# Kernel optimization log

Measured on AMD Instinct MI355X. Metric: run time of the kernel, lower is better.

## Reference

```python
import jax, jax.numpy as jnp
import numpy as np

BS, SL, H, DE, DT = 32, 512, 1024, 1024, 64


def setup_inputs() -> dict:
    key = jax.random.key(0)
    ks = jax.random.split(key, 12)
    cas_emb = jax.random.normal(ks[0], (BS, SL, DE), jnp.float32)
    # prefix (length) mask: position i valid iff i < length_b
    lengths = jax.random.randint(ks[1], (BS,), SL // 4, SL + 1)
    cas_mask = (jnp.arange(SL)[None, :] < lengths[:, None]).astype(jnp.float32)[..., None]
    time_weight = jax.random.uniform(ks[2], (BS, SL, DT), jnp.float32)
    s = 0.02
    return {
        "cas_emb": cas_emb,
        "cas_mask": cas_mask,
        "time_weight": time_weight,
        "W1": jax.random.normal(ks[3], (DE, H), jnp.float32) * s,
        "b1": jnp.zeros((H,), jnp.float32),
        "Wh": jax.random.normal(ks[4], (H, H), jnp.float32) * s,
        "bh": jnp.zeros((H,), jnp.float32),
        "Wt": jax.random.normal(ks[5], (H, H), jnp.float32) * s,
        "bt": jnp.zeros((H,), jnp.float32),
        "Wg": jax.random.normal(ks[6], (2 * H, H), jnp.float32) * s,
        "bg": jnp.zeros((H,), jnp.float32),
        "Wm1": jax.random.normal(ks[7], (H, H), jnp.float32) * s,
        "bm1": jnp.zeros((H,), jnp.float32),
        "Wti": jax.random.normal(ks[8], (DT, H), jnp.float32) * s,
        "bti": jnp.zeros((H,), jnp.float32),
        "Wm2": jax.random.normal(ks[9], (H, 1), jnp.float32) * s,
        "bm2": jnp.zeros((1,), jnp.float32),
    }


def reference(cas_emb, cas_mask, time_weight, W1, b1, Wh, bh, Wt, bt, Wg, bg,
              Wm1, bm1, Wti, bti, Wm2, bm2):
    NEG = jnp.float32(-1e30)
    sl = cas_emb.shape[1]
    # --- user2user: directional masked self-attention + fusion gate ---
    # attention_mask[b,i,j] = (i > j) and cas_mask[b,j]
    direction = (jnp.arange(sl)[:, None] > jnp.arange(sl)[None, :])  # [sl,sl]
    attn_mask = (direction[None] & (cas_mask[..., 0][:, None, :] > 0)).astype(cas_emb.dtype)  # [bs,sl,sl]
    cas_hidden = jax.nn.elu(cas_emb @ W1 + b1) * cas_mask  # [bs,sl,H]
    head = cas_hidden @ Wh + bh
    tail = cas_hidden @ Wt + bt
    logits = jnp.einsum('bih,bjh->bij', head, tail) + (1.0 - attn_mask) * NEG
    score = jax.nn.softmax(logits, axis=-1) * attn_mask  # renormalized-masked softmax
    depend = jnp.einsum('bij,bjh->bih', score, cas_hidden)
    gate = jax.nn.sigmoid(jnp.concatenate([cas_hidden, depend], axis=-1) @ Wg + bg)
    encoding = (gate * cas_hidden + (1.0 - gate) * depend) * cas_mask  # [bs,sl,H]
    # --- user2cas: time-weighted attention pooling ---
    map1 = jax.nn.elu(encoding @ Wm1 + bm1)
    time_inf = jax.nn.elu(time_weight @ Wti + bti)
    map2 = (map1 * time_inf) @ Wm2 + bm2  # [bs,sl,1]
    a = jax.nn.softmax(map2 + NEG * (1.0 - cas_mask), axis=1) * cas_mask
    return a * encoding
```

## Files before the change

### kernel.cpp

```cpp
#include <hip/hip_runtime.h>
#include <math.h>


#define BSZ 32
#define SLEN 512
#define HD 1024
#define DEMB 1024
#define DTW 64

typedef __attribute__((ext_vector_type(8))) short short8;
typedef __attribute__((ext_vector_type(4))) float f32x4;
typedef unsigned short ushort_t;

__device__ __forceinline__ unsigned short f2bf(float x) {
    unsigned int u = __float_as_uint(x);
    u += 0x7FFFu + ((u >> 16) & 1u);
    return (unsigned short)(u >> 16);
}
__device__ __forceinline__ float bf2f(unsigned short h) {
    return __uint_as_float(((unsigned int)h) << 16);
}

__device__ __forceinline__ void gload16(const void* g, void* l) {
    __builtin_amdgcn_global_load_lds((const __attribute__((address_space(1))) unsigned int*)g,
                                     (__attribute__((address_space(3))) unsigned int*)l,
                                     16, 0, 0);
}

template<int ACT, int MSK, int ACC, int WF32, int WBF16, int MODE, int EPI,
         int KCAP = 0, int SKIP = 0>
__global__ __launch_bounds__(256, 4)
void mgemm(const ushort_t* __restrict__ AH, const ushort_t* __restrict__ AL,
           long long ldA, long long bsA,
           const ushort_t* __restrict__ BH, const ushort_t* __restrict__ BL,
           long long ldB, long long bsB,
           const float* __restrict__ bias, const float* __restrict__ rowmask,
           long long mskb,
           float* __restrict__ C, long long ldC, long long bsC,
           ushort_t* __restrict__ OH, ushort_t* __restrict__ OL,
           long long ldO, long long bsO,
           int M, int N, int K,
           const float* __restrict__ f_tinf, const float* __restrict__ f_wm2,
           float* __restrict__ f_out)
{
    __shared__ alignas(16) ushort_t sAh[128 * 32];
    __shared__ alignas(16) ushort_t sAl[128 * 32];
    __shared__ alignas(16) ushort_t sBh[128 * 32];
    __shared__ alignas(16) ushort_t sBl[128 * 32];

    long long bz = blockIdx.z;
    int tid = threadIdx.x;
    int wv = tid >> 6, lane = tid & 63;
    int wr = wv >> 1, wc = wv & 1;
    int ln = lane & 15, qd = lane >> 4;

    int bx = blockIdx.x, by = blockIdx.y;
    if (MODE == 1) {
        int G = gridDim.x;
        int L = by * G + bx;
        int X = L & 7, S = L >> 3;
        bx = S % G;
        int t = S / G;
        by = ((t >> 1) * 8 + X) * 2 + (t & 1);
    }
    if (MODE == 2) {
        int l = blockIdx.x;
        if (l < 1)      { by = 0; bx = 0; }
        else if (l < 3) { by = 1; bx = l - 1; }
        else if (l < 6) { by = 2; bx = l - 3; }
        else            { by = 3; bx = l - 6; }
    }
    long long m0 = (long long)by * 128;
    long long n0 = (long long)bx * 128;

    if (SKIP) {
        int alive = __syncthreads_or(
            (tid < 128) && (rowmask[bz * mskb + m0 + tid] != 0.f));
        if (alive == 0) {
            if (SKIP == 1) {
                if (EPI == 2 || WBF16) {
                    ushort_t* OHb = OH + bz * bsO;
                    ushort_t* OLb = OL + bz * bsO;
                    short8 z = {};
                    #pragma unroll
                    for (int p = 0; p < 8; ++p) {
                        int idx = tid + p * 256;
                        long long o = (m0 + (idx >> 4)) * ldO + n0 + (idx & 15) * 8;
                        *(short8*)&OHb[o] = z;
                        *(short8*)&OLb[o] = z;
                    }
                }
                if (WF32) {
                    float* Cb = C + bz * bsC;
                    float4 z = make_float4(0.f, 0.f, 0.f, 0.f);
                    #pragma unroll
                    for (int p = 0; p < 16; ++p) {
                        int idx = tid + p * 256;
                        *(float4*)&Cb[(m0 + (idx >> 5)) * ldC + n0 + (idx & 31) * 4] = z;
                    }
                }
            }
            return;
        }
    }

    const ushort_t* gsrc;
    ushort_t* ldst;
    long long gld;
    if (wv == 0)      { gsrc = AH + bz * bsA + (m0 + (lane >> 2)) * ldA; ldst = sAh; gld = ldA; }
    else if (wv == 1) { gsrc = AL + bz * bsA + (m0 + (lane >> 2)) * ldA; ldst = sAl; gld = ldA; }
    else if (wv == 2) { gsrc = BH + bz * bsB + (n0 + (lane >> 2)) * ldB; ldst = sBh; gld = ldB; }
    else              { gsrc = BL + bz * bsB + (n0 + (lane >> 2)) * ldB; ldst = sBl; gld = ldB; }
    gsrc += (lane & 3) * 8;

    f32x4 acc[4][4] = {};

    int KL = K;
    if (KCAP) {
        long long kc = m0 + 128;
        if (kc < (long long)KL) KL = (int)kc;
    }

    for (int k0 = 0; k0 < KL; k0 += 32) {
        #pragma unroll
        for (int i = 0; i < 8; ++i)
            gload16(gsrc + (long long)(16 * i) * gld + k0, ldst + i * 512);
        __syncthreads();

        short8 fah[4], fal[4], fbh[4], fbl[4];
        #pragma unroll
        for (int i = 0; i < 4; ++i) {
            int ra = (64 * wr + 16 * i + ln) * 32 + qd * 8;
            int rb = (64 * wc + 16 * i + ln) * 32 + qd * 8;
            fah[i] = *(const short8*)&sAh[ra];
            fal[i] = *(const short8*)&sAl[ra];
            fbh[i] = *(const short8*)&sBh[rb];
            fbl[i] = *(const short8*)&sBl[rb];
        }
        #pragma unroll
        for (int i = 0; i < 4; ++i)
            #pragma unroll
            for (int j = 0; j < 4; ++j) {
                acc[i][j] = __builtin_amdgcn_mfma_f32_16x16x32_bf16(fah[i], fbh[j], acc[i][j], 0, 0, 0);
                acc[i][j] = __builtin_amdgcn_mfma_f32_16x16x32_bf16(fah[i], fbl[j], acc[i][j], 0, 0, 0);
                acc[i][j] = __builtin_amdgcn_mfma_f32_16x16x32_bf16(fal[i], fbh[j], acc[i][j], 0, 0, 0);
            }
        __syncthreads();
    }

    if (EPI == 1) {
        int Ni = N;
        #pragma unroll
        for (int i = 0; i < 4; ++i) {
            #pragma unroll
            for (int t = 0; t < 4; ++t) {
                int gm = (int)m0 + 64 * wr + 16 * i + qd * 4 + t;
                int tb = gm * Ni + (int)n0 + 64 * wc + ln;
                float part = 0.f;
                #pragma unroll
                for (int j = 0; j < 4; ++j) {
                    int gn = (int)n0 + 64 * wc + 16 * j + ln;
                    float x = acc[i][j][t] + bias[gn];
                    x = (x > 0.f) ? x : (expf(x) - 1.f);
                    part += x * f_tinf[tb + 16 * j] * f_wm2[gn];
                }
                part += __shfl_xor(part, 1);
                part += __shfl_xor(part, 2);
                part += __shfl_xor(part, 4);
                part += __shfl_xor(part, 8);
                if (ln == 0) atomicAdd(&f_out[gm], part);
            }
        }
        return;
    }

    if (EPI == 2) {
        int ldCi = (int)ldC, ldOi = (int)ldO, ldAi = (int)ldA;
        int nb = (int)n0 + 64 * wc + ln;
        #pragma unroll
        for (int i = 0; i < 4; ++i) {
            #pragma unroll
            for (int t = 0; t < 4; ++t) {
                int gm = (int)m0 + 64 * wr + 16 * i + qd * 4 + t;
                float mk = rowmask[gm];
                int cb = gm * ldCi + nb;
                int ob = gm * ldOi + nb;
                int ab = gm * ldAi + nb;
                #pragma unroll
                for (int j = 0; j < 4; ++j) {
                    float x = acc[i][j][t] + C[cb + 16 * j];
                    float g = 1.f / (1.f + expf(-x));
                    int o = ob + 16 * j;
                    float c = bf2f(OH[o]) + bf2f(OL[o]);
                    int ai = ab + 16 * j;
                    float d = bf2f(AH[ai]) + bf2f(AL[ai]);
                    float r = (g * c + (1.f - g) * d) * mk;
                    unsigned short h = f2bf(r);
                    OH[o] = h;
                    OL[o] = f2bf(r - bf2f(h));
                }
            }
        }
        return;
    }

    float* Cb = 0;
    ushort_t *OHb = 0, *OLb = 0;
    if (WF32 || ACC) Cb = C + bz * bsC;
    if (WBF16) { OHb = OH + bz * bsO; OLb = OL + bz * bsO; }

    #pragma unroll
    for (int i = 0; i < 4; ++i) {
        #pragma unroll
        for (int t = 0; t < 4; ++t) {
            long long gm = m0 + 64 * wr + 16 * i + qd * 4 + t;
            float mk = 1.f;
            if (MSK) mk = rowmask[gm];
            #pragma unroll
            for (int j = 0; j < 4; ++j) {
                long long gn = n0 + 64 * wc + 16 * j + ln;
                float x = acc[i][j][t];
                if (bias) x += bias[gn];
                if (ACC) x += Cb[gm * ldC + gn];
                if (ACT) x = (x > 0.f) ? x : (expf(x) - 1.f);
                if (MSK) x *= mk;
                if (WF32 || ACC) Cb[gm * ldC + gn] = x;
                if (WBF16) {
                    unsigned short h = f2bf(x);
                    OHb[gm * ldO + gn] = h;
                    OLb[gm * ldO + gn] = f2bf(x - bf2f(h));
                }
            }
        }
    }
}


__global__ __launch_bounds__(256)
void zero_k(float* __restrict__ p, long long n)
{
    long long i = blockIdx.x * 256LL + threadIdx.x;
    if (i < n) p[i] = 0.f;
}

__global__ __launch_bounds__(256)
void split_k(const float* __restrict__ x, ushort_t* __restrict__ h,
             ushort_t* __restrict__ l, long long n4)
{
    long long i = blockIdx.x * 256LL + threadIdx.x;
    long long stride = (long long)gridDim.x * 256LL;
    for (; i < n4; i += stride) {
        float4 v = ((const float4*)x)[i];
        ushort4 hv, lv;
        hv.x = f2bf(v.x); lv.x = f2bf(v.x - bf2f(hv.x));
        hv.y = f2bf(v.y); lv.y = f2bf(v.y - bf2f(hv.y));
        hv.z = f2bf(v.z); lv.z = f2bf(v.z - bf2f(hv.z));
        hv.w = f2bf(v.w); lv.w = f2bf(v.w - bf2f(hv.w));
        ((ushort4*)h)[i] = hv;
        ((ushort4*)l)[i] = lv;
    }
}

__global__ __launch_bounds__(256)
void tsplit_k(const float* __restrict__ X,
              ushort_t* __restrict__ Th, ushort_t* __restrict__ Tl,
              int K, int N)
{
    __shared__ float t[32][33];
    int n0 = blockIdx.x * 32, k0 = blockIdx.y * 32;
    int tx = threadIdx.x & 31, ty = threadIdx.x >> 5;
    #pragma unroll
    for (int p = 0; p < 32; p += 8)
        t[ty + p][tx] = X[(long long)(k0 + ty + p) * N + n0 + tx];
    __syncthreads();
    #pragma unroll
    for (int p = 0; p < 32; p += 8) {
        float v = t[tx][ty + p];
        unsigned short h = f2bf(v);
        long long o = (long long)(n0 + ty + p) * K + k0 + tx;
        Th[o] = h;
        Tl[o] = f2bf(v - bf2f(h));
    }
}

__global__ __launch_bounds__(256)
void trans_bf_k(const ushort_t* __restrict__ H, const ushort_t* __restrict__ L,
                ushort_t* __restrict__ TH, ushort_t* __restrict__ TL,
                int R, int C)
{
    __shared__ ushort_t sh[32][33];
    __shared__ ushort_t sl[32][33];
    long long b = blockIdx.z;
    long long ib = b * (long long)R * C;
    int c0 = blockIdx.x * 32, r0 = blockIdx.y * 32;
    int tx = threadIdx.x & 31, ty = threadIdx.x >> 5;
    #pragma unroll
    for (int p = 0; p < 32; p += 8) {
        long long src = ib + (long long)(r0 + ty + p) * C + c0 + tx;
        sh[ty + p][tx] = H[src];
        sl[ty + p][tx] = L[src];
    }
    __syncthreads();
    #pragma unroll
    for (int p = 0; p < 32; p += 8) {
        long long dst = ib + (long long)(c0 + ty + p) * R + r0 + tx;
        TH[dst] = sh[tx][ty + p];
        TL[dst] = sl[tx][ty + p];
    }
}

#define BM 64
#define BN 64
#define BK 16

template<int BT, int ACT, int ACC, int MSK>
__global__ __launch_bounds__(256)
void gemm_k(const float* __restrict__ A, long long sAb,
            const float* __restrict__ B, long long sBb,
            const float* __restrict__ bias,
            const float* __restrict__ rowmask,
            float* __restrict__ C, long long sCb,
            int M, int N, int K)
{
    int bz = blockIdx.z;
    A += (long long)bz * sAb;
    B += (long long)bz * sBb;
    C += (long long)bz * sCb;

    __shared__ float As[BK][BM + 4];
    __shared__ float Bs[BK][BN + 4];

    int tid = threadIdx.x;
    int tx = tid & 15;
    int ty = tid >> 4;
    int m0 = blockIdx.y * BM;
    int n0 = blockIdx.x * BN;

    int lm = tid >> 2;
    int lk = (tid & 3) << 2;
    int bk = tid >> 4;
    int bn = (tid & 15) << 2;

    float acc[4][4] = {};

    for (int k0 = 0; k0 < K; k0 += BK) {
        float4 av = *(const float4*)(A + (long long)(m0 + lm) * K + (k0 + lk));
        As[lk + 0][lm] = av.x;
        As[lk + 1][lm] = av.y;
        As[lk + 2][lm] = av.z;
        As[lk + 3][lm] = av.w;
        if (BT) {
            float4 bv = *(const float4*)(B + (long long)(n0 + lm) * K + (k0 + lk));
            Bs[lk + 0][lm] = bv.x;
            Bs[lk + 1][lm] = bv.y;
            Bs[lk + 2][lm] = bv.z;
            Bs[lk + 3][lm] = bv.w;
        } else {
            float4 bv = *(const float4*)(B + (long long)(k0 + bk) * N + (n0 + bn));
            *(float4*)&Bs[bk][bn] = bv;
        }
        __syncthreads();
        #pragma unroll
        for (int k = 0; k < BK; ++k) {
            float4 a4 = *(const float4*)&As[k][ty << 2];
            float4 b4 = *(const float4*)&Bs[k][tx << 2];
            float aa[4] = {a4.x, a4.y, a4.z, a4.w};
            float bb[4] = {b4.x, b4.y, b4.z, b4.w};
            #pragma unroll
            for (int i = 0; i < 4; ++i)
                #pragma unroll
                for (int j = 0; j < 4; ++j)
                    acc[i][j] = fmaf(aa[i], bb[j], acc[i][j]);
        }
        __syncthreads();
    }

    float bvals[4] = {0.f, 0.f, 0.f, 0.f};
    if (bias) {
        float4 b4 = *(const float4*)(bias + n0 + (tx << 2));
        bvals[0] = b4.x; bvals[1] = b4.y; bvals[2] = b4.z; bvals[3] = b4.w;
    }
    #pragma unroll
    for (int i = 0; i < 4; ++i) {
        int m = m0 + (ty << 2) + i;
        float mk = 1.f;
        if (MSK) mk = rowmask[m];
        float* cp = C + (long long)m * N + n0 + (tx << 2);
        float4 cv = make_float4(0.f, 0.f, 0.f, 0.f);
        if (ACC) cv = *(const float4*)cp;
        float v[4];
        #pragma unroll
        for (int j = 0; j < 4; ++j) {
            float x = acc[i][j] + bvals[j];
            if (ACC) x += (&cv.x)[j];
            if (ACT == 1) x = (x > 0.f) ? x : (expf(x) - 1.f);
            if (MSK) x *= mk;
            v[j] = x;
        }
        *(float4*)cp = make_float4(v[0], v[1], v[2], v[3]);
    }
}


__global__ __launch_bounds__(256)
void attn_softmax_bf_k(float* __restrict__ score, const float* __restrict__ mask)
{
    int bi = blockIdx.x;
    int b = bi >> 9;
    int i = bi & (SLEN - 1);
    float* row = score + (long long)bi * SLEN;
    ushort_t* us = (ushort_t*)row;
    const float* mrow = mask + (long long)b * SLEN;
    int tid = threadIdx.x;
    int j0 = tid, j1 = tid + 256;
    __shared__ float red[256];

    bool v0 = (j0 < i) && (mrow[j0] > 0.f);
    bool v1 = (j1 < i) && (mrow[j1] > 0.f);
    float x0 = v0 ? row[j0] : -INFINITY;
    float x1 = v1 ? row[j1] : -INFINITY;

    red[tid] = fmaxf(x0, x1); __syncthreads();
    for (int s = 128; s > 0; s >>= 1) {
        if (tid < s) red[tid] = fmaxf(red[tid], red[tid + s]);
        __syncthreads();
    }
    float m = red[0]; __syncthreads();

    float e0 = v0 ? expf(x0 - m) : 0.f;
    float e1 = v1 ? expf(x1 - m) : 0.f;
    red[tid] = e0 + e1; __syncthreads();
    for (int s = 128; s > 0; s >>= 1) {
        if (tid < s) red[tid] += red[tid + s];
        __syncthreads();
    }
    float sum = red[0];
    float inv = (sum > 0.f) ? (1.f / sum) : 0.f;
    float r0 = e0 * inv, r1 = e1 * inv;
    __syncthreads();
    unsigned short h0 = f2bf(r0), h1 = f2bf(r1);
    us[j0] = h0;       us[512 + j0] = f2bf(r0 - bf2f(h0));
    us[j1] = h1;       us[512 + j1] = f2bf(r1 - bf2f(h1));
}

__global__ __launch_bounds__(256)
void pool_softmax_k(const float* __restrict__ map2, const float* __restrict__ mask,
                    float* __restrict__ a)
{
    int b = blockIdx.x;
    const float* xr = map2 + (long long)b * SLEN;
    const float* mr = mask + (long long)b * SLEN;
    float* ar = a + (long long)b * SLEN;
    int tid = threadIdx.x;
    __shared__ float red[256];

    float lmax = -INFINITY;
    for (int j = tid; j < SLEN; j += 256)
        if (mr[j] > 0.f) lmax = fmaxf(lmax, xr[j]);
    red[tid] = lmax; __syncthreads();
    for (int s = 128; s > 0; s >>= 1) {
        if (tid < s) red[tid] = fmaxf(red[tid], red[tid + s]);
        __syncthreads();
    }
    float m = red[0]; __syncthreads();

    float lsum = 0.f;
    for (int j = tid; j < SLEN; j += 256) {
        float e = (mr[j] > 0.f) ? expf(xr[j] - m) : 0.f;
        ar[j] = e;
        lsum += e;
    }
    red[tid] = lsum; __syncthreads();
    for (int s = 128; s > 0; s >>= 1) {
        if (tid < s) red[tid] += red[tid + s];
        __syncthreads();
    }
    float inv = (red[0] > 0.f) ? (1.f / red[0]) : 0.f;
    for (int j = tid; j < SLEN; j += 256) ar[j] *= inv;
}

__global__ __launch_bounds__(256)
void final_bf_k(const ushort_t* __restrict__ encH, const ushort_t* __restrict__ encL,
                const float* __restrict__ a, float* __restrict__ out, long long n4)
{
    long long i = blockIdx.x * 256LL + threadIdx.x;
    long long stride = (long long)gridDim.x * 256LL;
    for (; i < n4; i += stride) {
        ushort4 h4 = ((const ushort4*)encH)[i];
        ushort4 l4 = ((const ushort4*)encL)[i];
        float av = a[i >> 8];
        float4 r;
        r.x = (bf2f(h4.x) + bf2f(l4.x)) * av;
        r.y = (bf2f(h4.y) + bf2f(l4.y)) * av;
        r.z = (bf2f(h4.z) + bf2f(l4.z)) * av;
        r.w = (bf2f(h4.w) + bf2f(l4.w)) * av;
        ((float4*)out)[i] = r;
    }
}

__global__ __launch_bounds__(256)
void attn_softmax_k(float* __restrict__ score, const float* __restrict__ mask)
{
    int bi = blockIdx.x;
    int b = bi >> 9;
    int i = bi & (SLEN - 1);
    float* row = score + (long long)bi * SLEN;
    const float* mrow = mask + (long long)b * SLEN;
    int tid = threadIdx.x;
    __shared__ float red[256];

    float lmax = -INFINITY;
    for (int j = tid; j < SLEN; j += 256)
        if (j < i && mrow[j] > 0.f) lmax = fmaxf(lmax, row[j]);
    red[tid] = lmax; __syncthreads();
    for (int s = 128; s > 0; s >>= 1) {
        if (tid < s) red[tid] = fmaxf(red[tid], red[tid + s]);
        __syncthreads();
    }
    float m = red[0]; __syncthreads();

    float lsum = 0.f;
    for (int j = tid; j < SLEN; j += 256) {
        bool valid = (j < i && mrow[j] > 0.f);
        float e = valid ? expf(row[j] - m) : 0.f;
        row[j] = e;
        lsum += e;
    }
    red[tid] = lsum; __syncthreads();
    for (int s = 128; s > 0; s >>= 1) {
        if (tid < s) red[tid] += red[tid + s];
        __syncthreads();
    }
    float sum = red[0];
    float inv = (sum > 0.f) ? (1.f / sum) : 0.f;
    for (int j = tid; j < SLEN; j += 256) row[j] *= inv;
}

__global__ __launch_bounds__(256)
void encode_k(const float* __restrict__ gp, float* __restrict__ ch,
              const float* __restrict__ dep, const float* __restrict__ mask,
              long long n4)
{
    long long i = blockIdx.x * 256LL + threadIdx.x;
    long long stride = (long long)gridDim.x * 256LL;
    for (; i < n4; i += stride) {
        float4 g4 = ((const float4*)gp)[i];
        float4 c4 = ((const float4*)ch)[i];
        float4 d4 = ((const float4*)dep)[i];
        float mk = mask[i >> 8];
        float4 r;
        float g = 1.f / (1.f + expf(-g4.x)); r.x = (g * c4.x + (1.f - g) * d4.x) * mk;
        g = 1.f / (1.f + expf(-g4.y)); r.y = (g * c4.y + (1.f - g) * d4.y) * mk;
        g = 1.f / (1.f + expf(-g4.z)); r.z = (g * c4.z + (1.f - g) * d4.z) * mk;
        g = 1.f / (1.f + expf(-g4.w)); r.w = (g * c4.w + (1.f - g) * d4.w) * mk;
        ((float4*)ch)[i] = r;
    }
}

__global__ __launch_bounds__(256)
void map2_k(const float* __restrict__ map1, const float* __restrict__ tinf,
            const float* __restrict__ Wm2, const float* __restrict__ bm2,
            float* __restrict__ out)
{
    long long r = blockIdx.x;
    const float* p1 = map1 + r * HD;
    const float* p2 = tinf + r * HD;
    int tid = threadIdx.x;
    float s = 0.f;
    for (int h = tid; h < HD; h += 256) s += p1[h] * p2[h] * Wm2[h];
    __shared__ float red[256];
    red[tid] = s; __syncthreads();
    for (int st = 128; st > 0; st >>= 1) {
        if (tid < st) red[tid] += red[tid + st];
        __syncthreads();
    }
    if (tid == 0) out[r] = red[0] + bm2[0];
}

__global__ __launch_bounds__(256)
void final_k(const float* __restrict__ enc, const float* __restrict__ a,
             float* __restrict__ out, long long n4)
{
    long long i = blockIdx.x * 256LL + threadIdx.x;
    long long stride = (long long)gridDim.x * 256LL;
    for (; i < n4; i += stride) {
        float4 e4 = ((const float4*)enc)[i];
        float av = a[i >> 8];
        ((float4*)out)[i] = make_float4(e4.x * av, e4.y * av, e4.z * av, e4.w * av);
    }
}


extern "C" void kernel_launch(void* const* d_in, const int* in_sizes, int n_in,
                              void* d_out, int out_size, void* d_ws, size_t ws_size,
                              hipStream_t stream)
{
    const float* cas_emb     = (const float*)d_in[0];
    const float* cas_mask    = (const float*)d_in[1];
    const float* time_weight = (const float*)d_in[2];
    const float* W1  = (const float*)d_in[3];
    const float* b1  = (const float*)d_in[4];
    const float* Wh  = (const float*)d_in[5];
    const float* bh  = (const float*)d_in[6];
    const float* Wt  = (const float*)d_in[7];
    const float* bt  = (const float*)d_in[8];
    const float* Wg  = (const float*)d_in[9];
    const float* bg  = (const float*)d_in[10];
    const float* Wm1 = (const float*)d_in[11];
    const float* bm1 = (const float*)d_in[12];
    const float* Wti = (const float*)d_in[13];
    const float* bti = (const float*)d_in[14];
    const float* Wm2 = (const float*)d_in[15];
    const float* bm2 = (const float*)d_in[16];
    float* out = (float*)d_out;

    const long long MR = (long long)BSZ * SLEN;
    const long long NH = MR * HD;
    const long long NS = (long long)BSZ * SLEN * SLEN;
    const long long WSZ = (long long)HD * DEMB;

    float* B0 = (float*)d_ws;
    float* B1 = B0 + NH;
    float* B2 = B1 + NH;
    float* m2 = B2 + NS;
    float* av = m2 + MR;
    size_t need = (size_t)(2 * NH + NS + 2 * MR) * 4;

    dim3 blk(256);
    const float* nofp = nullptr;
    float* nofpm = nullptr;

    if (ws_size >= need) {
        ushort_t* embH = (ushort_t*)B0; ushort_t* embL = embH + NH;
        ushort_t* chH  = (ushort_t*)B1; ushort_t* chL  = chH + NH;
        ushort_t* tmpH = (ushort_t*)B0; ushort_t* tmpL = tmpH + NH;
        ushort_t* chTH = (ushort_t*)B0; ushort_t* chTL = chTH + NH;
        ushort_t* depH = (ushort_t*)d_out; ushort_t* depL = depH + NH;
        float* Ssc  = B2;
        ushort_t* scB = (ushort_t*)B2;
        float* gp   = B0;
        float* tinf = (float*)d_out;
        ushort_t* Wb = (ushort_t*)B2;
        ushort_t* W1h = Wb,             * W1l  = Wb + WSZ;
        ushort_t* Whh = Wb + 2 * WSZ,   * Whl  = Wb + 3 * WSZ;
        ushort_t* Wth = Wb + 4 * WSZ,   * Wtl  = Wb + 5 * WSZ;
        ushort_t* WcTh = Wb + 6 * WSZ,  * WcTl = Wb + 7 * WSZ;
        ushort_t* Wgh  = Wb,            * Wgl  = Wb + 2 * WSZ;
        ushort_t* Wm1h = Wb + 4 * WSZ,  * Wm1l = Wb + 5 * WSZ;
        ushort_t* twH  = Wb + 6 * WSZ,  * twL  = Wb + 7 * WSZ;
        ushort_t* WtiTh = Wb + 8 * WSZ, * WtiTl = WtiTh + (long long)HD * DTW;

        tsplit_k<<<dim3(HD / 32, DEMB / 32), blk, 0, stream>>>(W1, W1h, W1l, DEMB, HD);
        split_k<<<dim3(1024), blk, 0, stream>>>(Wh, Whh, Whl, WSZ / 4);
        split_k<<<dim3(1024), blk, 0, stream>>>(Wt, Wth, Wtl, WSZ / 4);
        split_k<<<dim3(4096), blk, 0, stream>>>(cas_emb, embH, embL, NH / 4);

        mgemm<0, 0, 0, 0, 1, 0, 0><<<dim3(8, 8, 1), blk, 0, stream>>>(
            Wth, Wtl, HD, 0, Whh, Whl, HD, 0, nullptr, nullptr, 0,
            nullptr, 0, 0, WcTh, WcTl, HD, 0, HD, HD, HD, nofp, nofp, nofpm);
        mgemm<1, 1, 0, 0, 1, 1, 0, 0, 1><<<dim3(8, 128, 1), blk, 0, stream>>>(
            embH, embL, DEMB, 0, W1h, W1l, DEMB, 0, b1, cas_mask, 0,
            nullptr, 0, 0, chH, chL, HD, 0, (int)MR, HD, DEMB, nofp, nofp, nofpm);
        mgemm<0, 0, 0, 0, 1, 1, 0, 0, 1><<<dim3(8, 128, 1), blk, 0, stream>>>(
            chH, chL, HD, 0, WcTh, WcTl, HD, 0, nullptr, cas_mask, 0,
            nullptr, 0, 0, tmpH, tmpL, HD, 0, (int)MR, HD, HD, nofp, nofp, nofpm);
        mgemm<0, 0, 0, 1, 0, 2, 0, 0, 1><<<dim3(10, 1, BSZ), blk, 0, stream>>>(
            tmpH, tmpL, HD, (long long)SLEN * HD, chH, chL, HD, (long long)SLEN * HD,
            nullptr, cas_mask, SLEN, Ssc, SLEN, (long long)SLEN * SLEN,
            nullptr, nullptr, 0, 0, SLEN, SLEN, HD, nofp, nofp, nofpm);
        attn_softmax_bf_k<<<dim3(BSZ * SLEN), blk, 0, stream>>>(Ssc, cas_mask);
        trans_bf_k<<<dim3(HD / 32, SLEN / 32, BSZ), blk, 0, stream>>>(
            chH, chL, chTH, chTL, SLEN, HD);
        mgemm<0, 0, 0, 0, 1, 0, 0, 1, 1><<<dim3(8, 4, BSZ), blk, 0, stream>>>(
            scB, scB + 512, 1024, (long long)SLEN * 1024, chTH, chTL, SLEN, (long long)HD * SLEN,
            nullptr, cas_mask, SLEN, nullptr, 0, 0,
            depH, depL, HD, (long long)SLEN * HD, SLEN, HD, SLEN, nofp, nofp, nofpm);
        tsplit_k<<<dim3(HD / 32, 2048 / 32), blk, 0, stream>>>(Wg, Wgh, Wgl, 2048, HD);
        tsplit_k<<<dim3(HD / 32, HD / 32), blk, 0, stream>>>(Wm1, Wm1h, Wm1l, HD, HD);
        split_k<<<dim3(1024), blk, 0, stream>>>(time_weight, twH, twL, MR * DTW / 4);
        tsplit_k<<<dim3(HD / 32, DTW / 32), blk, 0, stream>>>(Wti, WtiTh, WtiTl, DTW, HD);
        mgemm<0, 0, 0, 1, 0, 1, 0, 0, 2><<<dim3(8, 128, 1), blk, 0, stream>>>(
            chH, chL, HD, 0, Wgh, Wgl, 2048, 0, bg, cas_mask, 0,
            gp, HD, 0, nullptr, nullptr, 0, 0, (int)MR, HD, HD, nofp, nofp, nofpm);
        mgemm<0, 0, 0, 0, 0, 1, 2, 0, 1><<<dim3(8, 128, 1), blk, 0, stream>>>(
            depH, depL, HD, 0, Wgh + 1024, Wgl + 1024, 2048, 0, nullptr, cas_mask, 0,
            gp, HD, 0, chH, chL, HD, 0, (int)MR, HD, HD, nofp, nofp, nofpm);
        mgemm<1, 0, 0, 1, 0, 1, 0><<<dim3(8, 128, 1), blk, 0, stream>>>(
            twH, twL, DTW, 0, WtiTh, WtiTl, DTW, 0, bti, nullptr, 0,
            tinf, HD, 0, nullptr, nullptr, 0, 0, (int)MR, HD, DTW, nofp, nofp, nofpm);
        zero_k<<<dim3(64), blk, 0, stream>>>(m2, MR);
        mgemm<0, 0, 0, 0, 0, 1, 1, 0, 2><<<dim3(8, 128, 1), blk, 0, stream>>>(
            chH, chL, HD, 0, Wm1h, Wm1l, HD, 0, bm1, cas_mask, 0,
            nullptr, 0, 0, nullptr, nullptr, 0, 0, (int)MR, HD, HD,
            tinf, Wm2, m2);
        pool_softmax_k<<<dim3(BSZ), blk, 0, stream>>>(m2, cas_mask, av);
        final_bf_k<<<dim3(8192), blk, 0, stream>>>(chH, chL, av, out, NH / 4);
    } else {
        float* S0 = B0;
        float* S1 = B1;
        float* S3 = B2;
        dim3 gBig(HD / BN, (int)(MR / BM), 1);
        gemm_k<0, 1, 0, 1><<<gBig, blk, 0, stream>>>(cas_emb, 0, W1, 0, b1, cas_mask, S0, 0, (int)MR, HD, DEMB);
        gemm_k<0, 0, 0, 0><<<gBig, blk, 0, stream>>>(S0, 0, Wh, 0, bh, nullptr, S1, 0, (int)MR, HD, HD);
        gemm_k<0, 0, 0, 0><<<gBig, blk, 0, stream>>>(S0, 0, Wt, 0, bt, nullptr, out, 0, (int)MR, HD, HD);
        gemm_k<1, 0, 0, 0><<<dim3(SLEN / BN, SLEN / BM, BSZ), blk, 0, stream>>>(
            S1, (long long)SLEN * HD, out, (long long)SLEN * HD, nullptr, nullptr,
            S3, (long long)SLEN * SLEN, SLEN, SLEN, HD);
        attn_softmax_k<<<dim3(BSZ * SLEN), blk, 0, stream>>>(S3, cas_mask);
        gemm_k<0, 0, 0, 0><<<dim3(HD / BN, SLEN / BM, BSZ), blk, 0, stream>>>(
            S3, (long long)SLEN * SLEN, S0, (long long)SLEN * HD, nullptr, nullptr,
            out, (long long)SLEN * HD, SLEN, HD, SLEN);
        gemm_k<0, 0, 0, 0><<<gBig, blk, 0, stream>>>(S0, 0, Wg, 0, bg, nullptr, S1, 0, (int)MR, HD, HD);
        gemm_k<0, 0, 1, 0><<<gBig, blk, 0, stream>>>(out, 0, Wg + (long long)HD * HD, 0, nullptr, nullptr, S1, 0, (int)MR, HD, HD);
        long long n4 = NH / 4;
        encode_k<<<dim3(8192), blk, 0, stream>>>(S1, S0, out, cas_mask, n4);
        gemm_k<0, 1, 0, 0><<<gBig, blk, 0, stream>>>(S0, 0, Wm1, 0, bm1, nullptr, S1, 0, (int)MR, HD, HD);
        gemm_k<0, 1, 0, 0><<<gBig, blk, 0, stream>>>(time_weight, 0, Wti, 0, bti, nullptr, out, 0, (int)MR, HD, DTW);
        map2_k<<<dim3((int)MR), blk, 0, stream>>>(S1, out, Wm2, bm2, m2);
        pool_softmax_k<<<dim3(BSZ), blk, 0, stream>>>(m2, cas_mask, av);
        final_k<<<dim3(8192), blk, 0, stream>>>(S0, av, out, n4);
    }
}
```

Baseline: 928.4 us.

## Fuse gate GEMM halves into one dual-K kernel, drop fp32 intermediate

The gate projection previously ran as two GEMMs: one computing cas_hidden@Wg[:H] into an fp32 buffer and a second adding depend@Wg[H:] with the gate epilogue. A DUAL mode now loops over both halves inside one kernel, switching the A source between cas_hidden and depend and offsetting into the B rows, so the fp32 partial buffer is neither written nor read back and one launch is removed. The skip test also switches from a block-wide __syncthreads_or to a per-wave __any over 128 mask entries. In exchange, skip now applies to the whole fused tile, and the epilogue reads bias instead of the stored partial.

```diff
diff --git a/kernel.cpp b/kernel.cpp
--- a/kernel.cpp
+++ b/kernel.cpp
@@ -28,7 +28,7 @@
 }
 
 template<int ACT, int MSK, int ACC, int WF32, int WBF16, int MODE, int EPI,
-         int KCAP = 0, int SKIP = 0>
+         int KCAP = 0, int SKIP = 0, int DUAL = 0>
 __global__ __launch_bounds__(256, 4)
 void mgemm(const ushort_t* __restrict__ AH, const ushort_t* __restrict__ AL,
            long long ldA, long long bsA,
@@ -74,9 +74,9 @@
     long long n0 = (long long)bx * 128;
 
     if (SKIP) {
-        int alive = __syncthreads_or(
-            (tid < 128) && (rowmask[bz * mskb + m0 + tid] != 0.f));
-        if (alive == 0) {
+        const float* mr = rowmask + bz * mskb + m0;
+        bool a = (mr[lane] != 0.f) || (mr[lane + 64] != 0.f);
+        if (!__any(a)) {
             if (SKIP == 1) {
                 if (EPI == 2 || WBF16) {
                     ushort_t* OHb = OH + bz * bsO;
@@ -121,31 +121,41 @@
         if (kc < (long long)KL) KL = (int)kc;
     }
 
-    for (int k0 = 0; k0 < KL; k0 += 32) {
-        #pragma unroll
-        for (int i = 0; i < 8; ++i)
-            gload16(gsrc + (long long)(16 * i) * gld + k0, ldst + i * 512);
-        __syncthreads();
-
-        short8 fah[4], fal[4], fbh[4], fbl[4];
-        #pragma unroll
-        for (int i = 0; i < 4; ++i) {
-            int ra = (64 * wr + 16 * i + ln) * 32 + qd * 8;
-            int rb = (64 * wc + 16 * i + ln) * 32 + qd * 8;
-            fah[i] = *(const short8*)&sAh[ra];
-            fal[i] = *(const short8*)&sAl[ra];
-            fbh[i] = *(const short8*)&sBh[rb];
-            fbl[i] = *(const short8*)&sBl[rb];
-        }
-        #pragma unroll
-        for (int i = 0; i < 4; ++i)
+    for (int half = 0; half < (DUAL ? 2 : 1); ++half) {
+        if (DUAL && wv < 2) {
+            const ushort_t* base = (wv == 0) ? (half ? AH : OH) : (half ? AL : OL);
+            gld = half ? ldA : ldO;
+            gsrc = base + bz * (half ? bsA : bsO) + (m0 + (lane >> 2)) * gld
+                 + (lane & 3) * 8;
+        }
+        long long koff = (DUAL && wv >= 2) ? (long long)half * K : 0;
+
+        for (int k0 = 0; k0 < KL; k0 += 32) {
             #pragma unroll
-            for (int j = 0; j < 4; ++j) {
-                acc[i][j] = __builtin_amdgcn_mfma_f32_16x16x32_bf16(fah[i], fbh[j], acc[i][j], 0, 0, 0);
-                acc[i][j] = __builtin_amdgcn_mfma_f32_16x16x32_bf16(fah[i], fbl[j], acc[i][j], 0, 0, 0);
-                acc[i][j] = __builtin_amdgcn_mfma_f32_16x16x32_bf16(fal[i], fbh[j], acc[i][j], 0, 0, 0);
+            for (int i = 0; i < 8; ++i)
+                gload16(gsrc + (long long)(16 * i) * gld + k0 + koff, ldst + i * 512);
+            __syncthreads();
+
+            short8 fah[4], fal[4], fbh[4], fbl[4];
+            #pragma unroll
+            for (int i = 0; i < 4; ++i) {
+                int ra = (64 * wr + 16 * i + ln) * 32 + qd * 8;
+                int rb = (64 * wc + 16 * i + ln) * 32 + qd * 8;
+                fah[i] = *(const short8*)&sAh[ra];
+                fal[i] = *(const short8*)&sAl[ra];
+                fbh[i] = *(const short8*)&sBh[rb];
+                fbl[i] = *(const short8*)&sBl[rb];
             }
-        __syncthreads();
+            #pragma unroll
+            for (int i = 0; i < 4; ++i)
+                #pragma unroll
+                for (int j = 0; j < 4; ++j) {
+                    acc[i][j] = __builtin_amdgcn_mfma_f32_16x16x32_bf16(fah[i], fbh[j], acc[i][j], 0, 0, 0);
+                    acc[i][j] = __builtin_amdgcn_mfma_f32_16x16x32_bf16(fah[i], fbl[j], acc[i][j], 0, 0, 0);
+                    acc[i][j] = __builtin_amdgcn_mfma_f32_16x16x32_bf16(fal[i], fbh[j], acc[i][j], 0, 0, 0);
+                }
+            __syncthreads();
+        }
     }
 
     if (EPI == 1) {
@@ -175,7 +185,7 @@
     }
 
     if (EPI == 2) {
-        int ldCi = (int)ldC, ldOi = (int)ldO, ldAi = (int)ldA;
+        int ldOi = (int)ldO, ldAi = (int)ldA;
         int nb = (int)n0 + 64 * wc + ln;
         #pragma unroll
         for (int i = 0; i < 4; ++i) {
@@ -183,12 +193,11 @@
             for (int t = 0; t < 4; ++t) {
                 int gm = (int)m0 + 64 * wr + 16 * i + qd * 4 + t;
                 float mk = rowmask[gm];
-                int cb = gm * ldCi + nb;
                 int ob = gm * ldOi + nb;
                 int ab = gm * ldAi + nb;
                 #pragma unroll
                 for (int j = 0; j < 4; ++j) {
-                    float x = acc[i][j][t] + C[cb + 16 * j];
+                    float x = acc[i][j][t] + bias[nb + 16 * j];
                     float g = 1.f / (1.f + expf(-x));
                     int o = ob + 16 * j;
                     float c = bf2f(OH[o]) + bf2f(OL[o]);
@@ -638,7 +647,6 @@
         ushort_t* depH = (ushort_t*)d_out; ushort_t* depL = depH + NH;
         float* Ssc  = B2;
         ushort_t* scB = (ushort_t*)B2;
-        float* gp   = B0;
         float* tinf = (float*)d_out;
         ushort_t* Wb = (ushort_t*)B2;
         ushort_t* W1h = Wb,             * W1l  = Wb + WSZ;
@@ -679,12 +687,9 @@
         tsplit_k<<<dim3(HD / 32, HD / 32), blk, 0, stream>>>(Wm1, Wm1h, Wm1l, HD, HD);
         split_k<<<dim3(1024), blk, 0, stream>>>(time_weight, twH, twL, MR * DTW / 4);
         tsplit_k<<<dim3(HD / 32, DTW / 32), blk, 0, stream>>>(Wti, WtiTh, WtiTl, DTW, HD);
-        mgemm<0, 0, 0, 1, 0, 1, 0, 0, 2><<<dim3(8, 128, 1), blk, 0, stream>>>(
-            chH, chL, HD, 0, Wgh, Wgl, 2048, 0, bg, cas_mask, 0,
-            gp, HD, 0, nullptr, nullptr, 0, 0, (int)MR, HD, HD, nofp, nofp, nofpm);
-        mgemm<0, 0, 0, 0, 0, 1, 2, 0, 1><<<dim3(8, 128, 1), blk, 0, stream>>>(
-            depH, depL, HD, 0, Wgh + 1024, Wgl + 1024, 2048, 0, nullptr, cas_mask, 0,
-            gp, HD, 0, chH, chL, HD, 0, (int)MR, HD, HD, nofp, nofp, nofpm);
+        mgemm<0, 0, 0, 0, 0, 1, 2, 0, 1, 1><<<dim3(8, 128, 1), blk, 0, stream>>>(
+            depH, depL, HD, 0, Wgh, Wgl, 2048, 0, bg, cas_mask, 0,
+            nullptr, 0, 0, chH, chL, HD, 0, (int)MR, HD, HD, nofp, nofp, nofpm);
         mgemm<1, 0, 0, 1, 0, 1, 0><<<dim3(8, 128, 1), blk, 0, stream>>>(
             twH, twL, DTW, 0, WtiTh, WtiTl, DTW, 0, bti, nullptr, 0,
             tinf, HD, 0, nullptr, nullptr, 0, 0, (int)MR, HD, DTW, nofp, nofp, nofpm);
```

Result: no change. 942.0 us (+1.5%).
